# Kernel optimization log

Hardware: AMD Instinct MI355X
Metric: run time of the kernel (lower is better)

The kernel has to match this reference:

```python
import jax, jax.numpy as jnp
import numpy as np
from jax.scipy.special import logsumexp

PAD, SOS, EOS = 0, 2, 3
V, E, H, L, K = 30000, 128, 256, 2, 32   # vocab, embed, hidden, lstm layers, tags
B, T = 64, 512
HP = H // L                               # per-direction hidden size (PyTorch: hidden_sz//num_layer)


def setup_inputs() -> dict:
    key = jax.random.key(0)
    ks = jax.random.split(key, 20)
    # sorted-descending lengths (pack_padded_sequence requirement)
    lengths = jnp.sort(jax.random.randint(ks[0], (B,), T // 2, T + 1))[::-1]
    pos = jnp.arange(T)
    valid = pos[None, :] < lengths[:, None]
    x = jnp.where(valid, jax.random.randint(ks[1], (B, T), 4, V), PAD)
    y = jax.random.randint(ks[2], (B, T + 1), 4, K).at[:, 0].set(SOS)
    embed = jax.random.normal(ks[3], (V, E)) * 0.1
    s = 1.0 / np.sqrt(HP)
    u = lambda k, shape: jax.random.uniform(k, shape, minval=-s, maxval=s)
    p = {}
    i = 4
    for l, din in [(0, E), (1, 2 * HP)]:
        for d in 'fb':
            p['wi_l%d%s' % (l, d)] = u(ks[i], (4 * HP, din)); i += 1
            p['wh_l%d%s' % (l, d)] = u(ks[i], (4 * HP, HP)); i += 1
            p['b_l%d%s' % (l, d)] = u(ks[i], (4 * HP,)); i += 1
    so = 1.0 / np.sqrt(H)
    w_out = jax.random.uniform(ks[i], (K, H), minval=-so, maxval=so); i += 1
    b_out = jax.random.uniform(ks[i], (K,), minval=-so, maxval=so); i += 1
    trans = jax.random.normal(ks[i], (K, K))
    trans = trans.at[SOS, :].set(-10000.0)
    trans = trans.at[:, EOS].set(-10000.0)
    trans = trans.at[:, PAD].set(-10000.0)
    trans = trans.at[PAD, :].set(-10000.0)
    trans = trans.at[PAD, EOS].set(0.0)
    trans = trans.at[PAD, PAD].set(0.0)
    return {'x': x, 'y': y, 'embed': embed, **p, 'w_out': w_out, 'b_out': b_out, 'trans': trans}


def _lstm_dir(xs, wi, wh, b):
    # xs: [T, B, D] -> hidden states [T, B, HP]; PyTorch gate order i, f, g, o
    bsz = xs.shape[1]
    def step(carry, xt):
        h, c = carry
        z = xt @ wi.T + h @ wh.T + b
        i, f, g, o = jnp.split(z, 4, axis=-1)
        c = jax.nn.sigmoid(f) * c + jax.nn.sigmoid(i) * jnp.tanh(g)
        h = jax.nn.sigmoid(o) * jnp.tanh(c)
        return (h, c), h
    init = (jnp.zeros((bsz, HP), xs.dtype), jnp.zeros((bsz, HP), xs.dtype))
    _, hs = jax.lax.scan(step, init, xs)
    return hs


def _flip(a, lengths):
    # per-sequence reversal of valid prefix (matches packed-sequence reverse LSTM)
    pos = jnp.arange(a.shape[1])
    idx = jnp.where(pos[None, :] < lengths[:, None], lengths[:, None] - 1 - pos[None, :], pos[None, :])
    return jnp.take_along_axis(a, idx[:, :, None], axis=1)


def _bilstm_layer(inp, lengths, wif, whf, bf, wib, whb, bb):
    hf = _lstm_dir(inp.swapaxes(0, 1), wif, whf, bf).swapaxes(0, 1)
    hb = _flip(_lstm_dir(_flip(inp, lengths).swapaxes(0, 1), wib, whb, bb).swapaxes(0, 1), lengths)
    return jnp.concatenate([hf, hb], axis=-1)


def _forward(x, y, embed, wi_l0f, wh_l0f, b_l0f, wi_l0b, wh_l0b, b_l0b,
             wi_l1f, wh_l1f, b_l1f, wi_l1b, wh_l1b, b_l1b, w_out, b_out, trans):
    mask = (x > PAD).astype(jnp.float32)          # [B, T]
    lengths = mask.sum(1).astype(jnp.int32)       # [B]
    h = embed[x]                                  # [B, T, E]
    h = _bilstm_layer(h, lengths, wi_l0f, wh_l0f, b_l0f, wi_l0b, wh_l0b, b_l0b)
    h = _bilstm_layer(h, lengths, wi_l1f, wh_l1f, b_l1f, wi_l1b, wh_l1b, b_l1b)
    h = jnp.einsum('btd,kd->btk', h, w_out) + b_out   # emissions [B, T, K]
    h = h * mask[:, :, None]
    bsz = x.shape[0]
    # CRF partition function: sequential log-sum-exp recurrence
    init = jnp.full((bsz, K), -10000.0).at[:, SOS].set(0.0)
    def step(score, tb):
        h_t, m_t = tb                              # [B, K], [B]
        s = logsumexp(score[:, None, :] + h_t[:, :, None] + trans[None, :, :], axis=-1)
        return jnp.where(m_t[:, None] > 0, s, score), None
    score, _ = jax.lax.scan(step, init, (h.swapaxes(0, 1), mask.T))
    logZ = logsumexp(score + trans[EOS], axis=-1)
    # gold path score
    emit = jnp.take_along_axis(h, y[:, 1:, None], axis=2)[..., 0]  # [B, T]
    tr = trans[y[:, 1:], y[:, :-1]]                                 # [B, T]
    gold = ((emit + tr) * mask).sum(1)
    last_tag = jnp.take_along_axis(y, lengths[:, None], axis=1)[:, 0]
    gold = gold + trans[EOS, last_tag]
    return logZ - gold                              # [B] negative log-likelihood


def reference(x, y, embed, wi_l0f, wh_l0f, b_l0f, wi_l0b, wh_l0b, b_l0b,
              wi_l1f, wh_l1f, b_l1f, wi_l1b, wh_l1b, b_l1b, w_out, b_out, trans):
    return _forward(x, y, embed, wi_l0f, wh_l0f, b_l0f, wi_l0b, wh_l0b, b_l0b,
                    wi_l1f, wh_l1f, b_l1f, wi_l1b, wh_l1b, b_l1b, w_out, b_out, trans)
```

## Files before the change

### kernel.cpp

```cpp
#include <hip/hip_runtime.h>

typedef _Float16 half_t;
typedef _Float16 half2_t __attribute__((ext_vector_type(2)));
typedef _Float16 half4_t __attribute__((ext_vector_type(4)));
typedef _Float16 half8_t __attribute__((ext_vector_type(8)));
typedef float float4_t __attribute__((ext_vector_type(4)));

#define BB 64
#define TT 512
#define EE 128
#define HPP 128
#define KK 32
#define MTOT (BB*TT)
#define NWID 1024

__device__ __forceinline__ void lds_barrier() {
    asm volatile("s_waitcnt lgkmcnt(0)\n\ts_barrier" ::: "memory");
}

__device__ __forceinline__ float fast_sigmoid(float x) {
    return __builtin_amdgcn_rcpf(1.f + __expf(-x));
}
__device__ __forceinline__ float fast_tanh(float x) {
    return 1.f - 2.f * __builtin_amdgcn_rcpf(__expf(2.f * x) + 1.f);
}

__global__ void k_lengths(const int* __restrict__ x, int* __restrict__ lens) {
    __shared__ int cnt;
    if (threadIdx.x == 0) cnt = 0;
    __syncthreads();
    int local = 0;
    for (int t = threadIdx.x; t < TT; t += blockDim.x)
        local += (x[blockIdx.x * TT + t] > 0) ? 1 : 0;
    atomicAdd(&cnt, local);
    __syncthreads();
    if (threadIdx.x == 0) lens[blockIdx.x] = cnt;
}

__global__ void k_pack(const float* __restrict__ wi0f, const float* __restrict__ wi0b,
                       const float* __restrict__ wi1f, const float* __restrict__ wi1b,
                       const float* __restrict__ w_out,
                       half_t* __restrict__ WP0, half_t* __restrict__ WP1,
                       half_t* __restrict__ WO) {
    int idx = blockIdx.x * blockDim.x + threadIdx.x;
    int stride = gridDim.x * blockDim.x;
    const int n0 = NWID * EE;
    const int n1 = NWID * 256;
    for (int i = idx; i < n0; i += stride) {
        int j8 = i & 7; int ln = (i >> 3) & 63; int rest = i >> 9;
        int kc = rest & 3; int ntg = rest >> 2;
        int lr = ln & 15, lq = ln >> 4;
        int n = ntg * 16 + lr;
        int k = kc * 32 + lq * 8 + j8;
        float v = (n < 512) ? wi0f[n * 128 + k] : wi0b[(n - 512) * 128 + k];
        WP0[i] = (half_t)v;
    }
    for (int i = idx; i < n1; i += stride) {
        int j8 = i & 7; int ln = (i >> 3) & 63; int rest = i >> 9;
        int kc = rest & 7; int ntg = rest >> 3;
        int lr = ln & 15, lq = ln >> 4;
        int n = ntg * 16 + lr;
        int k = kc * 32 + lq * 8 + j8;
        float v = (n < 512) ? wi1f[n * 256 + k] : wi1b[(n - 512) * 256 + k];
        WP1[i] = (half_t)v;
    }
    for (int i = idx; i < KK * 256; i += stride)
        WO[i] = (half_t)w_out[i];
}

__global__ void k_embed(const int* __restrict__ x, const float* __restrict__ embed,
                        half_t* __restrict__ e16) {
    int bt = blockIdx.x * 16 + (threadIdx.x >> 4);
    int c  = (threadIdx.x & 15) * 8;
    int xi = x[bt];
    const float4* src = (const float4*)(embed + (size_t)xi * EE + c);
    float4 a = src[0], b = src[1];
    half8_t o;
    o[0] = (half_t)a.x; o[1] = (half_t)a.y; o[2] = (half_t)a.z; o[3] = (half_t)a.w;
    o[4] = (half_t)b.x; o[5] = (half_t)b.y; o[6] = (half_t)b.z; o[7] = (half_t)b.w;
    *(half8_t*)(e16 + (size_t)bt * EE + c) = o;
}

__global__ __launch_bounds__(256) void k_gemm(const half_t* __restrict__ A,
                                              const half_t* __restrict__ WP,
                                              const float* __restrict__ bias_f,
                                              const float* __restrict__ bias_b,
                                              half_t* __restrict__ C, int Kd) {
    const int KC = Kd >> 5;
    int wave = threadIdx.x >> 6;
    int lane = threadIdx.x & 63;
    int m0 = blockIdx.x * 64 + wave * 16;
    int dir = blockIdx.y >> 1;
    int cg  = blockIdx.y & 1;
    int lr = lane & 15;
    int lq = lane >> 4;

    float4_t acc[16];
    #pragma unroll
    for (int i = 0; i < 16; i++) acc[i] = (float4_t){0.f, 0.f, 0.f, 0.f};

    const half_t* Arow  = A + (size_t)(m0 + lr) * Kd + lq * 8;
    const int ntile0 = dir * 32 + cg * 4;
    const half_t* Wbase = WP + ((size_t)ntile0 * KC * 64 + lane) * 8;

    for (int kc = 0; kc < KC; kc++) {
        half8_t af = *(const half8_t*)(Arow + kc * 32);
        #pragma unroll
        for (int nt = 0; nt < 16; nt++) {
            int g = nt >> 2, sub = nt & 3;
            half8_t bf = *(const half8_t*)(Wbase + (((size_t)(g * 8 + sub) * KC + kc) << 9));
            acc[nt] = __builtin_amdgcn_mfma_f32_16x16x32_f16(af, bf, acc[nt], 0, 0, 0);
        }
    }

    const float* bias = dir ? bias_b : bias_f;
    char* Crow = (char*)C + dir * 1024 + (size_t)(cg * 64) * 8;
    #pragma unroll
    for (int sub = 0; sub < 4; sub++) {
        int cbase = cg * 64 + sub * 16 + lr;
        float b0 = bias[cbase];
        float b1 = bias[128 + cbase];
        float b2 = bias[256 + cbase];
        float b3 = bias[384 + cbase];
        #pragma unroll
        for (int i = 0; i < 4; i++) {
            int m = m0 + lq * 4 + i;
            half4_t o;
            o[0] = (half_t)(acc[0 * 4 + sub][i] + b0);
            o[1] = (half_t)(acc[1 * 4 + sub][i] + b1);
            o[2] = (half_t)(acc[2 * 4 + sub][i] + b2);
            o[3] = (half_t)(acc[3 * 4 + sub][i] + b3);
            *(half4_t*)(Crow + (size_t)m * 2048 + (sub * 16 + lr) * 8) = o;
        }
    }
}

__global__ __launch_bounds__(512, 1) void k_lstm(const half_t* __restrict__ zbuf,
                                                 const float* __restrict__ wh_f,
                                                 const float* __restrict__ wh_b,
                                                 const int* __restrict__ lens,
                                                 half_t* __restrict__ hout) {
    const int grp  = blockIdx.x >> 1;
    const int dir  = blockIdx.x & 1;
    const int tid  = threadIdx.x;
    const int wv   = tid >> 6;
    const int lane = tid & 63;
    const int q    = lane >> 4;
    const int col  = lane & 15;
    const int s    = col & 3;
    const int ii   = col >> 2;
    const int b    = grp * 4 + s;
    const int Lb   = lens[b];
    const int maxL = lens[grp * 4];
    const float* wh = dir ? wh_b : wh_f;

    __shared__ half_t hb[2][512];

    half8_t a0[4], a1[4], a2[4], a3[4];
    #pragma unroll
    for (int i = 0; i < 4; i++) {
        int r = wv * 64 + i * 16 + col;
        int orow = (r & 3) * 128 + (r >> 2);
        #pragma unroll
        for (int ck = 0; ck < 4; ck++) {
            const float4* src = (const float4*)(wh + (size_t)orow * 128 + ck * 32 + q * 8);
            float4 f0 = src[0], f1 = src[1];
            half8_t h8;
            h8[0] = (half_t)f0.x; h8[1] = (half_t)f0.y; h8[2] = (half_t)f0.z; h8[3] = (half_t)f0.w;
            h8[4] = (half_t)f1.x; h8[5] = (half_t)f1.y; h8[6] = (half_t)f1.z; h8[7] = (half_t)f1.w;
            if (i == 0) a0[ck] = h8;
            else if (i == 1) a1[ck] = h8;
            else if (i == 2) a2[ck] = h8;
            else a3[ck] = h8;
        }
    }

    hb[0][tid] = (half_t)0.f;

    const int cell = wv * 16 + ii * 4 + q;
    const int woff = (cell >> 5) * 128 + (s * 4 + ((cell >> 3) & 3)) * 8 + (cell & 7);
    const int roff = (s * 4 + q) * 8;

    const bool s1 = (ii == 1), s2 = (ii == 2), s3 = (ii == 3);

    float c = 0.f;
    const char* zb8  = (const char*)zbuf + dir * 1024;
    char*       hob8 = (char*)hout + dir * 256;

    const int zdelta = dir ? -2048 : 2048;
    const int hdelta = dir ? -512 : 512;

    int t0 = dir ? (Lb - 1) : 0;
    int t1 = dir ? (Lb - 2) : 1;
    half4_t z1 = *(const half4_t*)(zb8 + (unsigned)((b * TT + t0) * 2048 + cell * 8));
    half4_t z2 = *(const half4_t*)(zb8 + (unsigned)((b * TT + t1) * 2048 + cell * 8));

    int zoff = (b * TT + (dir ? (Lb - 3) : 2)) * 2048 + cell * 8;
    int hoff = (b * TT + t0) * 512 + cell * 2;
    const unsigned deadoff = (unsigned)((b * TT + 511) * 512 + cell * 2);

    __syncthreads();

    const int maxL2 = (maxL + 1) & ~1;

#define LSTM_STEP(RB, ZC, T)                                                      \
    {                                                                             \
        half8_t bf0 = *(const half8_t*)&hb[RB][roff];                             \
        half8_t bf1 = *(const half8_t*)&hb[RB][128 + roff];                       \
        half8_t bf2 = *(const half8_t*)&hb[RB][256 + roff];                       \
        half8_t bf3 = *(const half8_t*)&hb[RB][384 + roff];                       \
        float4_t A0 = (float4_t){0.f, 0.f, 0.f, 0.f};                             \
        float4_t A1 = (float4_t){0.f, 0.f, 0.f, 0.f};                             \
        float4_t A2 = (float4_t){0.f, 0.f, 0.f, 0.f};                             \
        float4_t A3 = (float4_t){0.f, 0.f, 0.f, 0.f};                             \
        A0 = __builtin_amdgcn_mfma_f32_16x16x32_f16(a0[0], bf0, A0, 0, 0, 0);     \
        A1 = __builtin_amdgcn_mfma_f32_16x16x32_f16(a1[0], bf0, A1, 0, 0, 0);     \
        A2 = __builtin_amdgcn_mfma_f32_16x16x32_f16(a2[0], bf0, A2, 0, 0, 0);     \
        A3 = __builtin_amdgcn_mfma_f32_16x16x32_f16(a3[0], bf0, A3, 0, 0, 0);     \
        A0 = __builtin_amdgcn_mfma_f32_16x16x32_f16(a0[1], bf1, A0, 0, 0, 0);     \
        A1 = __builtin_amdgcn_mfma_f32_16x16x32_f16(a1[1], bf1, A1, 0, 0, 0);     \
        A2 = __builtin_amdgcn_mfma_f32_16x16x32_f16(a2[1], bf1, A2, 0, 0, 0);     \
        A3 = __builtin_amdgcn_mfma_f32_16x16x32_f16(a3[1], bf1, A3, 0, 0, 0);     \
        A0 = __builtin_amdgcn_mfma_f32_16x16x32_f16(a0[2], bf2, A0, 0, 0, 0);     \
        A1 = __builtin_amdgcn_mfma_f32_16x16x32_f16(a1[2], bf2, A1, 0, 0, 0);     \
        A2 = __builtin_amdgcn_mfma_f32_16x16x32_f16(a2[2], bf2, A2, 0, 0, 0);     \
        A3 = __builtin_amdgcn_mfma_f32_16x16x32_f16(a3[2], bf2, A3, 0, 0, 0);     \
        A0 = __builtin_amdgcn_mfma_f32_16x16x32_f16(a0[3], bf3, A0, 0, 0, 0);     \
        A1 = __builtin_amdgcn_mfma_f32_16x16x32_f16(a1[3], bf3, A1, 0, 0, 0);     \
        A2 = __builtin_amdgcn_mfma_f32_16x16x32_f16(a2[3], bf3, A2, 0, 0, 0);     \
        A3 = __builtin_amdgcn_mfma_f32_16x16x32_f16(a3[3], bf3, A3, 0, 0, 0);     \
        float g0 = s1 ? A1[0] : (s2 ? A2[0] : (s3 ? A3[0] : A0[0]));              \
        float g1 = s1 ? A1[1] : (s2 ? A2[1] : (s3 ? A3[1] : A0[1]));              \
        float g2 = s1 ? A1[2] : (s2 ? A2[2] : (s3 ? A3[2] : A0[2]));              \
        float g3 = s1 ? A1[3] : (s2 ? A2[3] : (s3 ? A3[3] : A0[3]));              \
        float zi = g0 + (float)ZC[0];                                             \
        float zf = g1 + (float)ZC[1];                                             \
        float zg = g2 + (float)ZC[2];                                             \
        float zo = g3 + (float)ZC[3];                                             \
        ZC = *(const half4_t*)(zb8 + (unsigned)zoff);         \
        zoff += zdelta;                                                           \
        zoff = zoff < 0 ? 0 : zoff;                                               \
        float si = fast_sigmoid(zi);                                              \
        float sf = fast_sigmoid(zf);                                              \
        float so = fast_sigmoid(zo);                                              \
        float tg = fast_tanh(zg);                                                 \
        c = sf * c + si * tg;                                                     \
        float th = fast_tanh(c);                                                  \
        half_t hh = (half_t)(so * th);                                            \
        hb[RB ^ 1][woff] = hh;                                                    \
        unsigned soff = ((T) < Lb) ? (unsigned)hoff : deadoff;                    \
        *(half_t*)(hob8 + soff) = hh;                        \
        hoff += hdelta;                                                           \
        lds_barrier();                                                            \
    }

    for (int t = 0; t < maxL2; t += 2) {
        LSTM_STEP(0, z1, t)
        LSTM_STEP(1, z2, t + 1)
    }
#undef LSTM_STEP
}

__global__ __launch_bounds__(256) void k_logits(const half_t* __restrict__ h1,
                                                const half_t* __restrict__ WO,
                                                const float* __restrict__ b_out,
                                                float* __restrict__ logits) {
    int wave = threadIdx.x >> 6;
    int lane = threadIdx.x & 63;
    int m0 = blockIdx.x * 64 + wave * 16;
    int lr = lane & 15;
    int lq = lane >> 4;

    float4_t acc0 = (float4_t){0.f, 0.f, 0.f, 0.f};
    float4_t acc1 = (float4_t){0.f, 0.f, 0.f, 0.f};

    const half_t* Arow = h1 + (size_t)(m0 + lr) * 256 + lq * 8;
    const half_t* Brow = WO + (size_t)lr * 256 + lq * 8;

    #pragma unroll
    for (int k = 0; k < 256; k += 32) {
        half8_t af = *(const half8_t*)(Arow + k);
        half8_t b0 = *(const half8_t*)(Brow + k);
        half8_t b1 = *(const half8_t*)(Brow + 16 * 256 + k);
        acc0 = __builtin_amdgcn_mfma_f32_16x16x32_f16(af, b0, acc0, 0, 0, 0);
        acc1 = __builtin_amdgcn_mfma_f32_16x16x32_f16(af, b1, acc1, 0, 0, 0);
    }
    #pragma unroll
    for (int nt = 0; nt < 2; nt++) {
        int n = nt * 16 + lr;
        float bias = b_out[n];
        #pragma unroll
        for (int i = 0; i < 4; i++) {
            int m = m0 + lq * 4 + i;
            logits[(size_t)m * KK + n] = (nt == 0 ? acc0[i] : acc1[i]) + bias;
        }
    }
}

__global__ __launch_bounds__(64) void k_crf(const float* __restrict__ logits,
                                            const float* __restrict__ trans,
                                            const int* __restrict__ y,
                                            const int* __restrict__ lens,
                                            float* __restrict__ out) {
    int b = blockIdx.x;
    int lane = threadIdx.x;
    int k = lane & 31;
    __shared__ float TR[32][33];
    __shared__ __align__(16) float PS[32];

    for (int i = lane; i < 1024; i += 64) TR[i >> 5][i & 31] = trans[i];

    float et[32];
    const float* trow = trans + k * 32;
    #pragma unroll
    for (int j = 0; j < 32; j++) et[j] = __expf(trow[j]);
    __syncthreads();

    int Lb = lens[b];
    const int* yb = y + b * (TT + 1);
    const float* lgb = logits + (size_t)(b * TT) * KK;

    float g = 0.f;
    for (int t = lane; t < Lb; t += 64) {
        int yt = yb[t], yt1 = yb[t + 1];
        g += lgb[(size_t)t * KK + yt1] + TR[yt1][yt];
    }
    #pragma unroll
    for (int s = 1; s < 64; s <<= 1) g += __shfl_xor(g, s);
    float gold = g + TR[3][yb[Lb]];

    float score = lgb[k] + TR[k][2];

    for (int t = 1; t < Lb; t++) {
        float lg = lgb[(size_t)t * KK + k];
        float m = __builtin_bit_cast(float, __builtin_amdgcn_readlane(__builtin_bit_cast(int, score), 4));
        float P = __expf(score - m);
        if (lane < 32) PS[k] = P;
        float4 ps[8];
        #pragma unroll
        for (int j = 0; j < 8; j++) ps[j] = *(const float4*)&PS[j * 4];
        const float* psf = (const float*)ps;
        float a0 = 0.f, a1 = 0.f, a2 = 0.f, a3 = 0.f;
        #pragma unroll
        for (int j = 0; j < 8; j++) {
            a0 = fmaf(et[j], psf[j], a0);
            a1 = fmaf(et[j + 8], psf[j + 8], a1);
            a2 = fmaf(et[j + 16], psf[j + 16], a2);
            a3 = fmaf(et[j + 24], psf[j + 24], a3);
        }
        score = lg + m + __logf((a0 + a1) + (a2 + a3));
    }

    float v = score + TR[3][k];
    float m2 = v;
    #pragma unroll
    for (int s = 1; s < 32; s <<= 1) m2 = fmaxf(m2, __shfl_xor(m2, s));
    float e = __expf(v - m2);
    #pragma unroll
    for (int s = 1; s < 32; s <<= 1) e += __shfl_xor(e, s);
    float logZ = m2 + __logf(e);

    if (lane == 0) out[b] = logZ - gold;
}

extern "C" void kernel_launch(void* const* d_in, const int* in_sizes, int n_in,
                              void* d_out, int out_size, void* d_ws, size_t ws_size,
                              hipStream_t stream) {
    const int*   x      = (const int*)d_in[0];
    const int*   y      = (const int*)d_in[1];
    const float* embed  = (const float*)d_in[2];
    const float* wi_l0f = (const float*)d_in[3];
    const float* wh_l0f = (const float*)d_in[4];
    const float* b_l0f  = (const float*)d_in[5];
    const float* wi_l0b = (const float*)d_in[6];
    const float* wh_l0b = (const float*)d_in[7];
    const float* b_l0b  = (const float*)d_in[8];
    const float* wi_l1f = (const float*)d_in[9];
    const float* wh_l1f = (const float*)d_in[10];
    const float* b_l1f  = (const float*)d_in[11];
    const float* wi_l1b = (const float*)d_in[12];
    const float* wh_l1b = (const float*)d_in[13];
    const float* b_l1b  = (const float*)d_in[14];
    const float* w_out  = (const float*)d_in[15];
    const float* b_out  = (const float*)d_in[16];
    const float* trans  = (const float*)d_in[17];
    float* out = (float*)d_out;

    char* base = (char*)d_ws;
    size_t off = 0;
    auto take = [&](size_t bytes) -> char* {
        char* r = base + off;
        off = (off + bytes + 255) & ~(size_t)255;
        return r;
    };
    half_t* zA  = (half_t*)take((size_t)MTOT * NWID * 2);
    half_t* h0  = (half_t*)take((size_t)MTOT * 256 * 2);
    half_t* h1  = (half_t*)take((size_t)MTOT * 256 * 2);
    half_t* e16 = (half_t*)take((size_t)MTOT * EE * 2);
    float*  lg  = (float*)take((size_t)MTOT * KK * 4);
    half_t* WP0 = (half_t*)take((size_t)NWID * EE * 2);
    half_t* WP1 = (half_t*)take((size_t)NWID * 256 * 2);
    half_t* WO  = (half_t*)take((size_t)KK * 256 * 2);
    int*    lens = (int*)take(BB * 4);

    k_lengths<<<BB, 256, 0, stream>>>(x, lens);
    k_pack<<<256, 256, 0, stream>>>(wi_l0f, wi_l0b, wi_l1f, wi_l1b, w_out, WP0, WP1, WO);
    k_embed<<<MTOT / 16, 256, 0, stream>>>(x, embed, e16);
    k_gemm<<<dim3(MTOT / 64, 4), 256, 0, stream>>>(e16, WP0, b_l0f, b_l0b, zA, 128);
    k_lstm<<<32, 512, 0, stream>>>(zA, wh_l0f, wh_l0b, lens, h0);
    k_gemm<<<dim3(MTOT / 64, 4), 256, 0, stream>>>(h0, WP1, b_l1f, b_l1b, zA, 256);
    k_lstm<<<32, 512, 0, stream>>>(zA, wh_l1f, wh_l1b, lens, h1);
    k_logits<<<MTOT / 64, 256, 0, stream>>>(h1, WO, b_out, lg);
    k_crf<<<BB, 64, 0, stream>>>(lg, trans, y, lens, out);
}
```

Before: 909.5 us.

## Fuse embedding gather into layer-0 GEMM, halve LSTM block size, prefetch CRF logits

```diff
diff --git a/kernel.cpp b/kernel.cpp
--- a/kernel.cpp
+++ b/kernel.cpp
@@ -68,17 +68,64 @@
         WO[i] = (half_t)w_out[i];
 }
 
-__global__ void k_embed(const int* __restrict__ x, const float* __restrict__ embed,
-                        half_t* __restrict__ e16) {
-    int bt = blockIdx.x * 16 + (threadIdx.x >> 4);
-    int c  = (threadIdx.x & 15) * 8;
-    int xi = x[bt];
-    const float4* src = (const float4*)(embed + (size_t)xi * EE + c);
-    float4 a = src[0], b = src[1];
-    half8_t o;
-    o[0] = (half_t)a.x; o[1] = (half_t)a.y; o[2] = (half_t)a.z; o[3] = (half_t)a.w;
-    o[4] = (half_t)b.x; o[5] = (half_t)b.y; o[6] = (half_t)b.z; o[7] = (half_t)b.w;
-    *(half8_t*)(e16 + (size_t)bt * EE + c) = o;
+__global__ __launch_bounds__(256) void k_gemm0(const int* __restrict__ x,
+                                               const float* __restrict__ embed,
+                                               const half_t* __restrict__ WP,
+                                               const float* __restrict__ bias_f,
+                                               const float* __restrict__ bias_b,
+                                               half_t* __restrict__ C) {
+    const int KC = 4;
+    int wave = threadIdx.x >> 6;
+    int lane = threadIdx.x & 63;
+    int m0 = blockIdx.x * 64 + wave * 16;
+    int dir = blockIdx.y >> 1;
+    int cg  = blockIdx.y & 1;
+    int lr = lane & 15;
+    int lq = lane >> 4;
+
+    float4_t acc[16];
+    #pragma unroll
+    for (int i = 0; i < 16; i++) acc[i] = (float4_t){0.f, 0.f, 0.f, 0.f};
+
+    int xi = x[m0 + lr];
+    const float* erow = embed + (size_t)xi * EE + lq * 8;
+    const int ntile0 = dir * 32 + cg * 4;
+    const half_t* Wbase = WP + ((size_t)ntile0 * KC * 64 + lane) * 8;
+
+    for (int kc = 0; kc < KC; kc++) {
+        float4 f0 = *(const float4*)(erow + kc * 32);
+        float4 f1 = *(const float4*)(erow + kc * 32 + 4);
+        half8_t af;
+        af[0] = (half_t)f0.x; af[1] = (half_t)f0.y; af[2] = (half_t)f0.z; af[3] = (half_t)f0.w;
+        af[4] = (half_t)f1.x; af[5] = (half_t)f1.y; af[6] = (half_t)f1.z; af[7] = (half_t)f1.w;
+        #pragma unroll
+        for (int nt = 0; nt < 16; nt++) {
+            int g = nt >> 2, sub = nt & 3;
+            half8_t bf = *(const half8_t*)(Wbase + (((size_t)(g * 8 + sub) * KC + kc) << 9));
+            acc[nt] = __builtin_amdgcn_mfma_f32_16x16x32_f16(af, bf, acc[nt], 0, 0, 0);
+        }
+    }
+
+    const float* bias = dir ? bias_b : bias_f;
+    char* Crow = (char*)C + dir * 1024 + (size_t)(cg * 64) * 8;
+    #pragma unroll
+    for (int sub = 0; sub < 4; sub++) {
+        int cbase = cg * 64 + sub * 16 + lr;
+        float b0 = bias[cbase];
+        float b1 = bias[128 + cbase];
+        float b2 = bias[256 + cbase];
+        float b3 = bias[384 + cbase];
+        #pragma unroll
+        for (int i = 0; i < 4; i++) {
+            int m = m0 + lq * 4 + i;
+            half4_t o;
+            o[0] = (half_t)(acc[0 * 4 + sub][i] + b0);
+            o[1] = (half_t)(acc[1 * 4 + sub][i] + b1);
+            o[2] = (half_t)(acc[2 * 4 + sub][i] + b2);
+            o[3] = (half_t)(acc[3 * 4 + sub][i] + b3);
+            *(half4_t*)(Crow + (size_t)m * 2048 + (sub * 16 + lr) * 8) = o;
+        }
+    }
 }
 
 __global__ __launch_bounds__(256) void k_gemm(const half_t* __restrict__ A,
@@ -135,7 +182,7 @@
     }
 }
 
-__global__ __launch_bounds__(512, 1) void k_lstm(const half_t* __restrict__ zbuf,
+__global__ __launch_bounds__(256, 1) void k_lstm(const half_t* __restrict__ zbuf,
                                                  const float* __restrict__ wh_f,
                                                  const float* __restrict__ wh_b,
                                                  const int* __restrict__ lens,
@@ -156,10 +203,10 @@
 
     __shared__ half_t hb[2][512];
 
-    half8_t a0[4], a1[4], a2[4], a3[4];
-    #pragma unroll
-    for (int i = 0; i < 4; i++) {
-        int r = wv * 64 + i * 16 + col;
+    half8_t a0[4], a1[4], a2[4], a3[4], a4[4], a5[4], a6[4], a7[4];
+    #pragma unroll
+    for (int i = 0; i < 8; i++) {
+        int r = wv * 128 + i * 16 + col;
         int orow = (r & 3) * 128 + (r >> 2);
         #pragma unroll
         for (int ck = 0; ck < 4; ck++) {
@@ -171,19 +218,26 @@
             if (i == 0) a0[ck] = h8;
             else if (i == 1) a1[ck] = h8;
             else if (i == 2) a2[ck] = h8;
-            else a3[ck] = h8;
-        }
-    }
-
-    hb[0][tid] = (half_t)0.f;
-
-    const int cell = wv * 16 + ii * 4 + q;
-    const int woff = (cell >> 5) * 128 + (s * 4 + ((cell >> 3) & 3)) * 8 + (cell & 7);
+            else if (i == 3) a3[ck] = h8;
+            else if (i == 4) a4[ck] = h8;
+            else if (i == 5) a5[ck] = h8;
+            else if (i == 6) a6[ck] = h8;
+            else a7[ck] = h8;
+        }
+    }
+
+    #pragma unroll
+    for (int i = 0; i < 4; i++) ((half_t*)hb)[tid + i * 256] = (half_t)0.f;
+
+    const int c0 = wv * 32 + ii * 4 + q;
+    const int c1 = c0 + 16;
+    const int woff0 = (c0 >> 5) * 128 + (s * 4 + ((c0 >> 3) & 3)) * 8 + (c0 & 7);
+    const int woff1 = (c1 >> 5) * 128 + (s * 4 + ((c1 >> 3) & 3)) * 8 + (c1 & 7);
     const int roff = (s * 4 + q) * 8;
 
-    const bool s1 = (ii == 1), s2 = (ii == 2), s3 = (ii == 3);
-
-    float c = 0.f;
+    const bool i1 = (ii == 1), i2 = (ii == 2), i3 = (ii == 3);
+
+    float cA = 0.f, cB = 0.f;
     const char* zb8  = (const char*)zbuf + dir * 1024;
     char*       hob8 = (char*)hout + dir * 256;
 
@@ -192,71 +246,103 @@
 
     int t0 = dir ? (Lb - 1) : 0;
     int t1 = dir ? (Lb - 2) : 1;
-    half4_t z1 = *(const half4_t*)(zb8 + (unsigned)((b * TT + t0) * 2048 + cell * 8));
-    half4_t z2 = *(const half4_t*)(zb8 + (unsigned)((b * TT + t1) * 2048 + cell * 8));
-
-    int zoff = (b * TT + (dir ? (Lb - 3) : 2)) * 2048 + cell * 8;
-    int hoff = (b * TT + t0) * 512 + cell * 2;
-    const unsigned deadoff = (unsigned)((b * TT + 511) * 512 + cell * 2);
+    unsigned zo0 = (unsigned)((b * TT + t0) * 2048 + c0 * 8);
+    unsigned zo1 = (unsigned)((b * TT + t1) * 2048 + c0 * 8);
+    half4_t z1a = *(const half4_t*)(zb8 + zo0);
+    half4_t z1b = *(const half4_t*)(zb8 + zo0 + 128);
+    half4_t z2a = *(const half4_t*)(zb8 + zo1);
+    half4_t z2b = *(const half4_t*)(zb8 + zo1 + 128);
+
+    int zoff = (b * TT + (dir ? (Lb - 3) : 2)) * 2048 + c0 * 8;
+    int hoff = (b * TT + t0) * 512 + c0 * 2;
+    const unsigned deadoff = (unsigned)((b * TT + 511) * 512 + c0 * 2);
 
     __syncthreads();
 
     const int maxL2 = (maxL + 1) & ~1;
 
-#define LSTM_STEP(RB, ZC, T)                                                      \
+#define LSTM_STEP(RB, ZA, ZB, T)                                                  \
     {                                                                             \
         half8_t bf0 = *(const half8_t*)&hb[RB][roff];                             \
         half8_t bf1 = *(const half8_t*)&hb[RB][128 + roff];                       \
         half8_t bf2 = *(const half8_t*)&hb[RB][256 + roff];                       \
         half8_t bf3 = *(const half8_t*)&hb[RB][384 + roff];                       \
-        float4_t A0 = (float4_t){0.f, 0.f, 0.f, 0.f};                             \
-        float4_t A1 = (float4_t){0.f, 0.f, 0.f, 0.f};                             \
-        float4_t A2 = (float4_t){0.f, 0.f, 0.f, 0.f};                             \
-        float4_t A3 = (float4_t){0.f, 0.f, 0.f, 0.f};                             \
+        float4_t A0 = (float4_t){0.f,0.f,0.f,0.f}, A1 = (float4_t){0.f,0.f,0.f,0.f}; \
+        float4_t A2 = (float4_t){0.f,0.f,0.f,0.f}, A3 = (float4_t){0.f,0.f,0.f,0.f}; \
+        float4_t A4 = (float4_t){0.f,0.f,0.f,0.f}, A5 = (float4_t){0.f,0.f,0.f,0.f}; \
+        float4_t A6 = (float4_t){0.f,0.f,0.f,0.f}, A7 = (float4_t){0.f,0.f,0.f,0.f}; \
         A0 = __builtin_amdgcn_mfma_f32_16x16x32_f16(a0[0], bf0, A0, 0, 0, 0);     \
         A1 = __builtin_amdgcn_mfma_f32_16x16x32_f16(a1[0], bf0, A1, 0, 0, 0);     \
         A2 = __builtin_amdgcn_mfma_f32_16x16x32_f16(a2[0], bf0, A2, 0, 0, 0);     \
         A3 = __builtin_amdgcn_mfma_f32_16x16x32_f16(a3[0], bf0, A3, 0, 0, 0);     \
+        A4 = __builtin_amdgcn_mfma_f32_16x16x32_f16(a4[0], bf0, A4, 0, 0, 0);     \
+        A5 = __builtin_amdgcn_mfma_f32_16x16x32_f16(a5[0], bf0, A5, 0, 0, 0);     \
+        A6 = __builtin_amdgcn_mfma_f32_16x16x32_f16(a6[0], bf0, A6, 0, 0, 0);     \
+        A7 = __builtin_amdgcn_mfma_f32_16x16x32_f16(a7[0], bf0, A7, 0, 0, 0);     \
         A0 = __builtin_amdgcn_mfma_f32_16x16x32_f16(a0[1], bf1, A0, 0, 0, 0);     \
         A1 = __builtin_amdgcn_mfma_f32_16x16x32_f16(a1[1], bf1, A1, 0, 0, 0);     \
         A2 = __builtin_amdgcn_mfma_f32_16x16x32_f16(a2[1], bf1, A2, 0, 0, 0);     \
         A3 = __builtin_amdgcn_mfma_f32_16x16x32_f16(a3[1], bf1, A3, 0, 0, 0);     \
+        A4 = __builtin_amdgcn_mfma_f32_16x16x32_f16(a4[1], bf1, A4, 0, 0, 0);     \
+        A5 = __builtin_amdgcn_mfma_f32_16x16x32_f16(a5[1], bf1, A5, 0, 0, 0);     \
+        A6 = __builtin_amdgcn_mfma_f32_16x16x32_f16(a6[1], bf1, A6, 0, 0, 0);     \
+        A7 = __builtin_amdgcn_mfma_f32_16x16x32_f16(a7[1], bf1, A7, 0, 0, 0);     \
         A0 = __builtin_amdgcn_mfma_f32_16x16x32_f16(a0[2], bf2, A0, 0, 0, 0);     \
         A1 = __builtin_amdgcn_mfma_f32_16x16x32_f16(a1[2], bf2, A1, 0, 0, 0);     \
         A2 = __builtin_amdgcn_mfma_f32_16x16x32_f16(a2[2], bf2, A2, 0, 0, 0);     \
         A3 = __builtin_amdgcn_mfma_f32_16x16x32_f16(a3[2], bf2, A3, 0, 0, 0);     \
+        A4 = __builtin_amdgcn_mfma_f32_16x16x32_f16(a4[2], bf2, A4, 0, 0, 0);     \
+        A5 = __builtin_amdgcn_mfma_f32_16x16x32_f16(a5[2], bf2, A5, 0, 0, 0);     \
+        A6 = __builtin_amdgcn_mfma_f32_16x16x32_f16(a6[2], bf2, A6, 0, 0, 0);     \
+        A7 = __builtin_amdgcn_mfma_f32_16x16x32_f16(a7[2], bf2, A7, 0, 0, 0);     \
         A0 = __builtin_amdgcn_mfma_f32_16x16x32_f16(a0[3], bf3, A0, 0, 0, 0);     \
         A1 = __builtin_amdgcn_mfma_f32_16x16x32_f16(a1[3], bf3, A1, 0, 0, 0);     \
         A2 = __builtin_amdgcn_mfma_f32_16x16x32_f16(a2[3], bf3, A2, 0, 0, 0);     \
         A3 = __builtin_amdgcn_mfma_f32_16x16x32_f16(a3[3], bf3, A3, 0, 0, 0);     \
-        float g0 = s1 ? A1[0] : (s2 ? A2[0] : (s3 ? A3[0] : A0[0]));              \
-        float g1 = s1 ? A1[1] : (s2 ? A2[1] : (s3 ? A3[1] : A0[1]));              \
-        float g2 = s1 ? A1[2] : (s2 ? A2[2] : (s3 ? A3[2] : A0[2]));              \
-        float g3 = s1 ? A1[3] : (s2 ? A2[3] : (s3 ? A3[3] : A0[3]));              \
-        float zi = g0 + (float)ZC[0];                                             \
-        float zf = g1 + (float)ZC[1];                                             \
-        float zg = g2 + (float)ZC[2];                                             \
-        float zo = g3 + (float)ZC[3];                                             \
-        ZC = *(const half4_t*)(zb8 + (unsigned)zoff);         \
+        A4 = __builtin_amdgcn_mfma_f32_16x16x32_f16(a4[3], bf3, A4, 0, 0, 0);     \
+        A5 = __builtin_amdgcn_mfma_f32_16x16x32_f16(a5[3], bf3, A5, 0, 0, 0);     \
+        A6 = __builtin_amdgcn_mfma_f32_16x16x32_f16(a6[3], bf3, A6, 0, 0, 0);     \
+        A7 = __builtin_amdgcn_mfma_f32_16x16x32_f16(a7[3], bf3, A7, 0, 0, 0);     \
+        float g0 = i1 ? A1[0] : (i2 ? A2[0] : (i3 ? A3[0] : A0[0]));              \
+        float g1 = i1 ? A1[1] : (i2 ? A2[1] : (i3 ? A3[1] : A0[1]));              \
+        float g2 = i1 ? A1[2] : (i2 ? A2[2] : (i3 ? A3[2] : A0[2]));              \
+        float g3 = i1 ? A1[3] : (i2 ? A2[3] : (i3 ? A3[3] : A0[3]));              \
+        float h0_ = i1 ? A5[0] : (i2 ? A6[0] : (i3 ? A7[0] : A4[0]));             \
+        float h1_ = i1 ? A5[1] : (i2 ? A6[1] : (i3 ? A7[1] : A4[1]));             \
+        float h2_ = i1 ? A5[2] : (i2 ? A6[2] : (i3 ? A7[2] : A4[2]));             \
+        float h3_ = i1 ? A5[3] : (i2 ? A6[3] : (i3 ? A7[3] : A4[3]));             \
+        float ziA = g0 + (float)ZA[0];                                            \
+        float zfA = g1 + (float)ZA[1];                                            \
+        float zgA = g2 + (float)ZA[2];                                            \
+        float zoA = g3 + (float)ZA[3];                                            \
+        float ziB = h0_ + (float)ZB[0];                                           \
+        float zfB = h1_ + (float)ZB[1];                                           \
+        float zgB = h2_ + (float)ZB[2];                                           \
+        float zoB = h3_ + (float)ZB[3];                                           \
+        ZA = *(const half4_t*)(zb8 + (unsigned)zoff);             \
+        ZB = *(const half4_t*)(zb8 + (unsigned)zoff + 128);       \
         zoff += zdelta;                                                           \
         zoff = zoff < 0 ? 0 : zoff;                                               \
-        float si = fast_sigmoid(zi);                                              \
-        float sf = fast_sigmoid(zf);                                              \
-        float so = fast_sigmoid(zo);                                              \
-        float tg = fast_tanh(zg);                                                 \
-        c = sf * c + si * tg;                                                     \
-        float th = fast_tanh(c);                                                  \
-        half_t hh = (half_t)(so * th);                                            \
-        hb[RB ^ 1][woff] = hh;                                                    \
+        float siA = fast_sigmoid(ziA), sfA = fast_sigmoid(zfA);                   \
+        float soA = fast_sigmoid(zoA), tgA = fast_tanh(zgA);                      \
+        cA = sfA * cA + siA * tgA;                                                \
+        half_t hhA = (half_t)(soA * fast_tanh(cA));                               \
+        float siB = fast_sigmoid(ziB), sfB = fast_sigmoid(zfB);                   \
+        float soB = fast_sigmoid(zoB), tgB = fast_tanh(zgB);                      \
+        cB = sfB * cB + siB * tgB;                                                \
+        half_t hhB = (half_t)(soB * fast_tanh(cB));                               \
+        hb[RB ^ 1][woff0] = hhA;                                                  \
+        hb[RB ^ 1][woff1] = hhB;                                                  \
         unsigned soff = ((T) < Lb) ? (unsigned)hoff : deadoff;                    \
-        *(half_t*)(hob8 + soff) = hh;                        \
+        *(half_t*)(hob8 + soff) = hhA;                       \
+        *(half_t*)(hob8 + soff + 32) = hhB;         \
         hoff += hdelta;                                                           \
         lds_barrier();                                                            \
     }
 
     for (int t = 0; t < maxL2; t += 2) {
-        LSTM_STEP(0, z1, t)
-        LSTM_STEP(1, z2, t + 1)
+        LSTM_STEP(0, z1a, z1b, t)
+        LSTM_STEP(1, z2a, z2b, t + 1)
     }
 #undef LSTM_STEP
 }
@@ -331,8 +417,12 @@
 
     float score = lgb[k] + TR[k][2];
 
+    const float* lgp = lgb + KK + k;
+    float lg_cur = *lgp;
     for (int t = 1; t < Lb; t++) {
-        float lg = lgb[(size_t)t * KK + k];
+        float lg_use = lg_cur;
+        lgp += KK;
+        lg_cur = *lgp;
         float m = __builtin_bit_cast(float, __builtin_amdgcn_readlane(__builtin_bit_cast(int, score), 4));
         float P = __expf(score - m);
         if (lane < 32) PS[k] = P;
@@ -348,7 +438,7 @@
             a2 = fmaf(et[j + 16], psf[j + 16], a2);
             a3 = fmaf(et[j + 24], psf[j + 24], a3);
         }
-        score = lg + m + __logf((a0 + a1) + (a2 + a3));
+        score = lg_use + m + __logf((a0 + a1) + (a2 + a3));
     }
 
     float v = score + TR[3][k];
@@ -396,7 +486,6 @@
     half_t* zA  = (half_t*)take((size_t)MTOT * NWID * 2);
     half_t* h0  = (half_t*)take((size_t)MTOT * 256 * 2);
     half_t* h1  = (half_t*)take((size_t)MTOT * 256 * 2);
-    half_t* e16 = (half_t*)take((size_t)MTOT * EE * 2);
     float*  lg  = (float*)take((size_t)MTOT * KK * 4);
     half_t* WP0 = (half_t*)take((size_t)NWID * EE * 2);
     half_t* WP1 = (half_t*)take((size_t)NWID * 256 * 2);
@@ -405,11 +494,10 @@
 
     k_lengths<<<BB, 256, 0, stream>>>(x, lens);
     k_pack<<<256, 256, 0, stream>>>(wi_l0f, wi_l0b, wi_l1f, wi_l1b, w_out, WP0, WP1, WO);
-    k_embed<<<MTOT / 16, 256, 0, stream>>>(x, embed, e16);
-    k_gemm<<<dim3(MTOT / 64, 4), 256, 0, stream>>>(e16, WP0, b_l0f, b_l0b, zA, 128);
-    k_lstm<<<32, 512, 0, stream>>>(zA, wh_l0f, wh_l0b, lens, h0);
+    k_gemm0<<<dim3(MTOT / 64, 4), 256, 0, stream>>>(x, embed, WP0, b_l0f, b_l0b, zA);
+    k_lstm<<<32, 256, 0, stream>>>(zA, wh_l0f, wh_l0b, lens, h0);
     k_gemm<<<dim3(MTOT / 64, 4), 256, 0, stream>>>(h0, WP1, b_l1f, b_l1b, zA, 256);
-    k_lstm<<<32, 512, 0, stream>>>(zA, wh_l1f, wh_l1b, lens, h1);
+    k_lstm<<<32, 256, 0, stream>>>(zA, wh_l1f, wh_l1b, lens, h1);
     k_logits<<<MTOT / 64, 256, 0, stream>>>(h1, WO, b_out, lg);
     k_crf<<<BB, 64, 0, stream>>>(lg, trans, y, lens, out);
 }
```

Result: slower. 1.147 ms (+26.1%).
